# Kernel optimization log

Hardware: AMD Instinct MI355X
Metric: run time of the kernel (lower is better)

The kernel has to match this reference:

```python
import jax, jax.numpy as jnp
import numpy as np

B, S, E, H, D = 4, 2048, 1024, 8, 128
EPS = 1e-5


def _ln(x, g, b):
    m = jnp.mean(x, axis=-1, keepdims=True)
    v = jnp.mean((x - m) ** 2, axis=-1, keepdims=True)
    return (x - m) * jax.lax.rsqrt(v + EPS) * g + b


def _xavier(k, shape, fan_in, fan_out):
    lim = float(np.sqrt(6.0 / (fan_in + fan_out)))
    return jax.random.uniform(k, shape, jnp.float32, -lim, lim)


def setup_inputs() -> dict:
    key = jax.random.key(0)
    ks = jax.random.split(key, 10)
    return {
        "x": jax.random.normal(ks[0], (B, S, E), jnp.float32),
        # embedding_to_z: Linear(E, H*D); stored as [E, H*D] for x @ W
        "W_ez": _xavier(ks[1], (E, H * D), E, H * D),
        "b_ez": jnp.zeros((H * D,), jnp.float32),
        "U_h": _xavier(ks[2], (H, D, D), D, D),
        "U_z": _xavier(ks[3], (H, D, D), D, D),
        "b_u": jnp.zeros((H, D), jnp.float32),
        "out_shaper": _xavier(ks[4], (H, D, D), D, D),
        # shared per-step state LayerNorm
        "lns_g": jnp.ones((D,), jnp.float32),
        "lns_b": jnp.zeros((D,), jnp.float32),
        # per-head FFN: LayerNorm(D) -> Linear(D,D) -> GELU -> Linear(D,E)
        "ff_ln_g": jnp.ones((H, D), jnp.float32),
        "ff_ln_b": jnp.zeros((H, D), jnp.float32),
        "ff_W1": _xavier(ks[5], (H, D, D), D, D),
        "ff_b1": jnp.zeros((H, D), jnp.float32),
        "ff_W2": _xavier(ks[6], (H, D, E), D, E),
        "ff_b2": jnp.zeros((H, E), jnp.float32),
        # layer_attention_weights: Linear(E, 1)
        "w_att": _xavier(ks[7], (E,), E, 1),
        "b_att": jnp.zeros((), jnp.float32),
        # output LayerNorm
        "lno_g": jnp.ones((E,), jnp.float32),
        "lno_b": jnp.zeros((E,), jnp.float32),
    }


def reference(x, W_ez, b_ez, U_h, U_z, b_u, out_shaper, lns_g, lns_b,
              ff_ln_g, ff_ln_b, ff_W1, ff_b1, ff_W2, ff_b2,
              w_att, b_att, lno_g, lno_b):
    b, s, _ = x.shape
    h, d = U_h.shape[0], U_h.shape[1]
    # z tokens: [B,S,H,D]
    z = jnp.tanh((x @ W_ez + b_ez).reshape(b, s, h, d))
    # torch.einsum('bhd,hdd->bhd') takes the DIAGONAL of the second operand
    uh_diag = jnp.einsum('hii->hi', U_h)          # [H,D]
    uz_diag = jnp.einsum('hii->hi', U_z)          # [H,D]
    os_diag = jnp.einsum('hii->hi', out_shaper)   # [H,D]

    def step(h_prev, z_t):
        # h_prev, z_t: [B,H,D]
        u = jax.nn.sigmoid(h_prev * uh_diag + z_t * uz_diag + b_u)
        h_new = u * h_prev + (1.0 - u) * z_t
        h_new = _ln(h_new, lns_g, lns_b)
        return h_new, h_new

    h0 = jnp.zeros((b, h, d), x.dtype)
    _, states = jax.lax.scan(step, h0, jnp.swapaxes(z, 0, 1))  # [S,B,H,D]
    states = jnp.swapaxes(states, 0, 1)                         # [B,S,H,D]

    shaped = states * os_diag                                   # diag einsum
    hln = _ln(shaped, ff_ln_g, ff_ln_b)                         # per-head LN
    h1 = jax.nn.gelu(jnp.einsum('bshd,hde->bshe', hln, ff_W1) + ff_b1,
                     approximate=False)                         # [B,S,H,D]
    ff_out = jnp.einsum('bshd,hde->bshe', h1, ff_W2) + ff_b2    # [B,S,H,E]

    scores = jax.nn.softmax(jnp.einsum('bshe,e->bsh', ff_out, w_att) + b_att,
                            axis=2)                             # over heads
    weighted = jnp.einsum('bshe,bsh->bse', ff_out, scores)      # [B,S,E]
    return _ln(weighted, lno_g, lno_b)
```

## Files before the change

### kernel.cpp

```cpp
#include <hip/hip_runtime.h>
#include <hip/hip_bf16.h>
#include <math.h>

#define BB 4
#define SS 2048
#define EE 1024
#define HH 8
#define DD 128
#define BSR (BB*SS)
#define HD  (HH*DD)
#define LNEPS 1e-5f
#define LOG2E 1.4426950408889634f

#define NCHUNK 16
#define CHS    128
#define NZT    512
#define TPC    64
#define NTICK  (NZT + NCHUNK*TPC)
#define NWORKER 224
#define NSLOT  6
#define SLOTF  (BB*CHS*1024)

#define FSCAN 16
#define FB    32
#define FD    96
#define FE    160
#define FZ    224

typedef __attribute__((ext_vector_type(8))) short bf16x8;
typedef __attribute__((ext_vector_type(4))) float f32x4;

__device__ __forceinline__ ushort f2bf(float f) {
    union { float f; unsigned u; } c{f};
    unsigned r = c.u + 0x7fff + ((c.u >> 16) & 1);
    return (ushort)(r >> 16);
}
__device__ __forceinline__ float bf2f(ushort b) {
    union { unsigned u; float f; } c{(unsigned)b << 16};
    return c.f;
}

typedef __attribute__((address_space(1))) const unsigned int GUI;
typedef __attribute__((address_space(3))) unsigned int LUI;
__device__ __forceinline__ void gl_lds16(const ushort* g, ushort* l) {
    __builtin_amdgcn_global_load_lds((GUI*)g, (LUI*)l, 16, 0, 0);
}

__device__ __forceinline__ float dpp_add(float x, const int ctrl) {
    int y;
    switch (ctrl) {
        case 0x111: y = __builtin_amdgcn_update_dpp(0, __float_as_int(x), 0x111, 0xf, 0xf, true); break;
        case 0x112: y = __builtin_amdgcn_update_dpp(0, __float_as_int(x), 0x112, 0xf, 0xf, true); break;
        case 0x114: y = __builtin_amdgcn_update_dpp(0, __float_as_int(x), 0x114, 0xf, 0xf, true); break;
        case 0x118: y = __builtin_amdgcn_update_dpp(0, __float_as_int(x), 0x118, 0xf, 0xf, true); break;
        case 0x142: y = __builtin_amdgcn_update_dpp(0, __float_as_int(x), 0x142, 0xf, 0xf, true); break;
        default:    y = __builtin_amdgcn_update_dpp(0, __float_as_int(x), 0x143, 0xf, 0xf, true); break;
    }
    return x + __int_as_float(y);
}

__device__ __forceinline__ float wave_sum64(float x) {
    x = dpp_add(x, 0x111);
    x = dpp_add(x, 0x112);
    x = dpp_add(x, 0x114);
    x = dpp_add(x, 0x118);
    x = dpp_add(x, 0x142);
    x = dpp_add(x, 0x143);
    return __int_as_float(__builtin_amdgcn_readlane(__float_as_int(x), 63));
}

__device__ __forceinline__ unsigned flag_peek(unsigned* f) {
    return __hip_atomic_fetch_add(f, 0u, __ATOMIC_RELAXED, __HIP_MEMORY_SCOPE_AGENT);
}
__device__ __forceinline__ void wait_ge(unsigned* f, unsigned tgt) {
    if (threadIdx.x == 0) {
        while (flag_peek(f) < tgt) __builtin_amdgcn_s_sleep(16);
        __builtin_amdgcn_fence(__ATOMIC_ACQUIRE, "agent");
    }
    __syncthreads();
}
__device__ __forceinline__ void wave_wait_ge(unsigned* f, unsigned tgt) {
    unsigned v = 0;
    for (;;) {
        if (threadIdx.x == 0) v = flag_peek(f);
        v = __shfl(v, 0, 64);
        if (v >= tgt) break;
        __builtin_amdgcn_s_sleep(8);
    }
    __builtin_amdgcn_fence(__ATOMIC_ACQUIRE, "agent");
}
__device__ __forceinline__ void done_inc(unsigned* f) {
    __syncthreads();
    if (threadIdx.x == 0) {
        __builtin_amdgcn_fence(__ATOMIC_RELEASE, "agent");
        __hip_atomic_fetch_add(f, 1u, __ATOMIC_RELAXED, __HIP_MEMORY_SCOPE_AGENT);
    }
}
__device__ __forceinline__ unsigned done_inc_ret(unsigned* f, unsigned* sh) {
    __syncthreads();
    if (threadIdx.x == 0) {
        __builtin_amdgcn_fence(__ATOMIC_RELEASE, "agent");
        *sh = __hip_atomic_fetch_add(f, 1u, __ATOMIC_RELAXED, __HIP_MEMORY_SCOPE_AGENT);
    }
    __syncthreads();
    return *sh;
}

__global__ __launch_bounds__(256)
void convx2_k(const float* __restrict__ x,
              ushort* __restrict__ hi, ushort* __restrict__ lo)
{
    const size_t idx = ((size_t)blockIdx.x * 256 + threadIdx.x) * 4;
    const float4 v = *(const float4*)(x + idx);
    ushort4 oh, ol;
    oh.x = f2bf(v.x); ol.x = f2bf(v.x - bf2f(oh.x));
    oh.y = f2bf(v.y); ol.y = f2bf(v.y - bf2f(oh.y));
    oh.z = f2bf(v.z); ol.z = f2bf(v.z - bf2f(oh.z));
    oh.w = f2bf(v.w); ol.w = f2bf(v.w - bf2f(oh.w));
    *(ushort4*)(hi + idx) = oh;
    *(ushort4*)(lo + idx) = ol;
}

__global__ __launch_bounds__(256)
void prepall_k(const float* __restrict__ W_ez,
               ushort* __restrict__ Wth, ushort* __restrict__ Wtl,
               const float* __restrict__ W2, ushort* __restrict__ W2t,
               const float* __restrict__ W1, ushort* __restrict__ W1t,
               const float* __restrict__ w_att, const float* __restrict__ b2,
               const float* __restrict__ b_att,
               const float* __restrict__ Uh, const float* __restrict__ Uz,
               const float* __restrict__ Os,
               float* __restrict__ q, float* __restrict__ c,
               float* __restrict__ uh_d, float* __restrict__ uz_d,
               float* __restrict__ os_d, unsigned* __restrict__ flags)
{
    __shared__ float tile[32][33];
    const int blk = blockIdx.x;
    if (blk == 2434) {
        flags[threadIdx.x] = 0;
        return;
    }
    const int tx = threadIdx.x & 31, ty = threadIdx.x >> 5;
    if (blk < 1024) {
        const int k0 = (blk >> 5) * 32, n0 = (blk & 31) * 32;
        #pragma unroll
        for (int i = 0; i < 4; ++i)
            tile[ty + i*8][tx] = W_ez[(size_t)(k0 + ty + i*8) * 1024 + n0 + tx];
        __syncthreads();
        #pragma unroll
        for (int i = 0; i < 4; ++i) {
            const float v = tile[tx][ty + i*8];
            const ushort h = f2bf(v);
            Wth[(size_t)(n0 + ty + i*8) * 1024 + k0 + tx] = h;
            Wtl[(size_t)(n0 + ty + i*8) * 1024 + k0 + tx] = f2bf(v - bf2f(h));
        }
    } else if (blk < 2048) {
        const int b2i = blk - 1024;
        const int k0 = (b2i >> 5) * 32, n0 = (b2i & 31) * 32;
        #pragma unroll
        for (int i = 0; i < 4; ++i)
            tile[ty + i*8][tx] = W2[(size_t)(k0 + ty + i*8) * 1024 + n0 + tx];
        __syncthreads();
        #pragma unroll
        for (int i = 0; i < 4; ++i)
            W2t[(size_t)(n0 + ty + i*8) * 1024 + k0 + tx] = f2bf(tile[tx][ty + i*8]);
    } else if (blk < 2176) {
        const int idx = blk - 2048;
        const int hh = idx >> 4;
        const int k0 = (idx & 3) * 32, n0 = ((idx >> 2) & 3) * 32;
        const float* Wb = W1 + (size_t)hh * DD * DD;
        ushort*      Wtb = W1t + (size_t)hh * DD * DD;
        #pragma unroll
        for (int i = 0; i < 4; ++i)
            tile[ty + i*8][tx] = Wb[(size_t)(k0 + ty + i*8) * DD + n0 + tx];
        __syncthreads();
        #pragma unroll
        for (int i = 0; i < 4; ++i)
            Wtb[(size_t)(n0 + ty + i*8) * DD + k0 + tx] = f2bf(tile[tx][ty + i*8]);
    } else {
        const int gid  = (blk - 2176) * 256 + threadIdx.x;
        const int wave = gid >> 6, lane = gid & 63;
        if (wave < HD) {
            const float* wp = W2 + (size_t)wave * EE;
            float p = 0.f;
            for (int e = lane; e < EE; e += 64) p = fmaf(wp[e], w_att[e], p);
            #pragma unroll
            for (int off = 32; off > 0; off >>= 1) p += __shfl_xor(p, off, 64);
            if (lane == 0) {
                q[wave] = p;
                const int h = wave >> 7, d = wave & 127;
                uh_d[wave] = Uh[(size_t)h*DD*DD + (size_t)d*DD + d];
                uz_d[wave] = Uz[(size_t)h*DD*DD + (size_t)d*DD + d];
                os_d[wave] = Os[(size_t)h*DD*DD + (size_t)d*DD + d];
            }
        } else if (wave < HD + HH) {
            const int h = wave - HD;
            const float* bp = b2 + (size_t)h * EE;
            float p = 0.f;
            for (int e = lane; e < EE; e += 64) p = fmaf(bp[e], w_att[e], p);
            #pragma unroll
            for (int off = 32; off > 0; off >>= 1) p += __shfl_xor(p, off, 64);
            if (lane == 0) c[h] = p + b_att[0];
        }
    }
}

__global__ __launch_bounds__(256)
void pipeline_k(float* z,
                const ushort* xbh, const ushort* xbl,
                const ushort* __restrict__ Wzh, const ushort* __restrict__ Wzl,
                const float* __restrict__ b_ez,
                const float* __restrict__ uh_d, const float* __restrict__ uz_d,
                const float* __restrict__ b_u,
                const float* __restrict__ lns_g, const float* __restrict__ lns_b,
                ushort* stb,
                const float* __restrict__ os_d,
                const float* __restrict__ ffg, const float* __restrict__ ffb,
                const ushort* __restrict__ W1t, const float* __restrict__ ff_b1,
                const float* __restrict__ qv, const float* __restrict__ cv,
                ushort* __restrict__ h1b, float* __restrict__ logits,
                const ushort* __restrict__ W2t, const float* __restrict__ ff_b2,
                float* __restrict__ wslots,
                const float* __restrict__ lno_g, const float* __restrict__ lno_b,
                float* __restrict__ out,
                unsigned* __restrict__ flags)
{
    __shared__ ushort ldspad[20480];
    if (flags[255] == 0xdeadbeefu)
        ((volatile ushort*)ldspad)[threadIdx.x] = 1;

    if (blockIdx.x < 32) {
        if (threadIdx.x >= 64) return;
        __builtin_amdgcn_s_setprio(3);
        const int bh = blockIdx.x;
        const int b = bh >> 3, h = bh & 7;
        const int l = threadIdx.x;
        const int d0 = 2*l, d1 = d0 + 1;

        const float uhn0 = -uh_d[h*DD+d0] * LOG2E, uhn1 = -uh_d[h*DD+d1] * LOG2E;
        const float uzn0 = -uz_d[h*DD+d0] * LOG2E, uzn1 = -uz_d[h*DD+d1] * LOG2E;
        const float bun0 = -b_u [h*DD+d0] * LOG2E, bun1 = -b_u [h*DD+d1] * LOG2E;
        const float g0  = lns_g[d0], g1 = lns_g[d1];
        const float be0 = lns_b[d0], be1 = lns_b[d1];
        const float A0 = g0 * uhn0, A1 = g1 * uhn1;
        const float bunB0 = fmaf(be0, uhn0, bun0);
        const float bunB1 = fmaf(be1, uhn1, bun1);

        const float* zp = z + ((size_t)b * SS * HH + h) * DD + d0;
        unsigned* op = (unsigned*)(stb + (size_t)b * SS * HD + h * DD) + l;

        wave_wait_ge(&flags[FZ + 0], 32);

        const int CH = 8;
        float2 zc[CH], zn[CH];
        float pb0[CH], pb1[CH];
        #pragma unroll
        for (int i = 0; i < CH; ++i) zc[i] = *(const float2*)(zp + (size_t)i*HD);
        #pragma unroll
        for (int i = 0; i < CH; ++i) {
            pb0[i] = fmaf(zc[i].x, uzn0, bunB0);
            pb1[i] = fmaf(zc[i].y, uzn1, bunB1);
        }

        float r_c, wp0, wp1, W0, W1, dv0, dv1;

#define PACK_STORE(HP0, HP1, OFF) do {                                       \
            const unsigned pu0 = __float_as_uint(HP0) + 0x8000u;             \
            const unsigned pu1 = __float_as_uint(HP1) + 0x8000u;             \
            op[(size_t)(OFF) * (HD/2)] =                                     \
                __builtin_amdgcn_perm(pu1, pu0, 0x07060302u);                \
        } while (0)

#define SCAN_STEP(ZX, ZY, PB0v, PB1v, ZNX, ZNY, OFF) do {                    \
            const float t0 = fmaf(r_c, W0, (PB0v));                          \
            const float t1 = fmaf(r_c, W1, (PB1v));                          \
            const float e0 = __builtin_amdgcn_exp2f(t0);                     \
            const float e1 = __builtin_amdgcn_exp2f(t1);                     \
            const float u0 = __builtin_amdgcn_rcpf(1.f + e0);                \
            const float u1 = __builtin_amdgcn_rcpf(1.f + e1);                \
            const float hn0 = fmaf(u0, dv0, (ZX));                           \
            const float hn1 = fmaf(u1, dv1, (ZY));                           \
            const float s1 = wave_sum64(hn0 + hn1);                          \
            const float s2 = wave_sum64(fmaf(hn0, hn0, hn1*hn1));            \
            const float m   = s1 * (1.f/128.f);                              \
            const float var = fmaf(s2, 1.f/128.f, -m*m);                     \
            r_c = __builtin_amdgcn_rsqf(var + LNEPS);                        \
            wp0 = hn0 - m; wp1 = hn1 - m;                                    \
            W0 = wp0 * A0; W1 = wp1 * A1;                                    \
            const float hp0 = fmaf(wp0, r_c * g0, be0);                      \
            const float hp1 = fmaf(wp1, r_c * g1, be1);                      \
            PACK_STORE(hp0, hp1, OFF);                                       \
            dv0 = hp0 - (ZNX); dv1 = hp1 - (ZNY);                            \
        } while (0)

        {
            const float z0 = zc[0].x, z1 = zc[0].y;
            const float t0 = fmaf(z0, uzn0, bun0);
            const float t1 = fmaf(z1, uzn1, bun1);
            const float e0 = __builtin_amdgcn_exp2f(t0);
            const float e1 = __builtin_amdgcn_exp2f(t1);
            const float u0 = __builtin_amdgcn_rcpf(1.f + e0);
            const float u1 = __builtin_amdgcn_rcpf(1.f + e1);
            const float hn0 = fmaf(u0, -z0, z0);
            const float hn1 = fmaf(u1, -z1, z1);
            const float s1 = wave_sum64(hn0 + hn1);
            const float s2 = wave_sum64(fmaf(hn0, hn0, hn1*hn1));
            const float m   = s1 * (1.f/128.f);
            const float var = fmaf(s2, 1.f/128.f, -m*m);
            r_c = __builtin_amdgcn_rsqf(var + LNEPS);
            wp0 = hn0 - m; wp1 = hn1 - m;
            W0 = wp0 * A0; W1 = wp1 * A1;
            const float hp0 = fmaf(wp0, r_c * g0, be0);
            const float hp1 = fmaf(wp1, r_c * g1, be1);
            PACK_STORE(hp0, hp1, 0);
            dv0 = hp0 - zc[1].x; dv1 = hp1 - zc[1].y;
        }

        #pragma unroll
        for (int i = 0; i < CH; ++i)
            zn[i] = *(const float2*)(zp + (size_t)(CH+i)*HD);
        #pragma unroll
        for (int i = 1; i < CH; ++i) {
            const float znx = (i+1 < CH) ? zc[i+1].x : zn[0].x;
            const float zny = (i+1 < CH) ? zc[i+1].y : zn[0].y;
            SCAN_STEP(zc[i].x, zc[i].y, pb0[i], pb1[i], znx, zny, i);
        }
        #pragma unroll
        for (int i = 0; i < CH; ++i) {
            zc[i] = zn[i];
            pb0[i] = fmaf(zn[i].x, uzn0, bunB0);
            pb1[i] = fmaf(zn[i].y, uzn1, bunB1);
        }

        for (int s0 = CH; s0 < SS; s0 += CH) {
            if (s0 + CH < SS) {
                if (((s0 + CH) & (CHS-1)) == 0)
                    wave_wait_ge(&flags[FZ + ((s0 + CH) >> 7)], 32);
                #pragma unroll
                for (int i = 0; i < CH; ++i)
                    zn[i] = *(const float2*)(zp + (size_t)(s0+CH+i)*HD);
            } else {
                #pragma unroll
                for (int i = 0; i < CH; ++i) zn[i] = make_float2(0.f, 0.f);
            }
            #pragma unroll
            for (int i = 0; i < CH; ++i) {
                const float znx = (i+1 < CH) ? zc[i+1].x : zn[0].x;
                const float zny = (i+1 < CH) ? zc[i+1].y : zn[0].y;
                SCAN_STEP(zc[i].x, zc[i].y, pb0[i], pb1[i], znx, zny, s0 + i);
            }
            #pragma unroll
            for (int i = 0; i < CH; ++i) {
                zc[i] = zn[i];
                pb0[i] = fmaf(zn[i].x, uzn0, bunB0);
                pb1[i] = fmaf(zn[i].y, uzn1, bunB1);
            }
            if ((s0 & (CHS-1)) == CHS - CH) {
                if (threadIdx.x == 0) {
                    __builtin_amdgcn_fence(__ATOMIC_RELEASE, "agent");
                    __hip_atomic_fetch_add(&flags[FSCAN + (s0 >> 7)], 1u,
                                           __ATOMIC_RELAXED, __HIP_MEMORY_SCOPE_AGENT);
                }
            }
        }
#undef SCAN_STEP
#undef PACK_STORE
        return;
    }

    __shared__ ushort ApS[4*128*32];
    __shared__ ushort Bsm[128*32];
    __shared__ float  sLDS[128][8];
    __shared__ float  lpart[128][2];
    __shared__ unsigned s_tk, s_old;
    const int tid = threadIdx.x;
    const int lane = tid & 63, w = tid >> 6;
    const int wr = w >> 1, wc = w & 1;
    const int lr = lane >> 2;
    const int lc = (lane & 3) ^ (lr & 3);
    const int quad = lane >> 4;
    const int fr   = lane & 15;
    const int fchk = (quad ^ (lane & 3)) * 8;

    for (;;) {
        __syncthreads();
        if (tid == 0) s_tk = __hip_atomic_fetch_add(&flags[0], 1u,
                               __ATOMIC_RELAXED, __HIP_MEMORY_SCOPE_AGENT);
        __syncthreads();
        const unsigned tk = s_tk;
        if (tk >= NTICK) return;

        if (tk < NZT) {
            const int zc = (int)(tk >> 5), zb = (int)((tk >> 3) & 3), zy = (int)(tk & 7);
            const int row0 = zb*SS + zc*CHS, col0 = zy*128;
            ushort* AH = ApS;
            ushort* AL = ApS + 4096;
            ushort* BH = ApS + 8192;
            ushort* BL = ApS + 12288;
            const size_t aoff0 = (size_t)(row0 +      w*16 + lr) * 1024 + lc*8;
            const size_t aoff1 = (size_t)(row0 + 64 + w*16 + lr) * 1024 + lc*8;
            const size_t boff0 = (size_t)(col0 +      w*16 + lr) * 1024 + lc*8;
            const size_t boff1 = (size_t)(col0 + 64 + w*16 + lr) * 1024 + lc*8;
            ushort* AH0 = AH + (     w*16) * 32;  ushort* AH1 = AH + (64 + w*16) * 32;
            ushort* AL0 = AL + (     w*16) * 32;  ushort* AL1 = AL + (64 + w*16) * 32;
            ushort* BH0 = BH + (     w*16) * 32;  ushort* BH1 = BH + (64 + w*16) * 32;
            ushort* BL0 = BL + (     w*16) * 32;  ushort* BL1 = BL + (64 + w*16) * 32;

            f32x4 acc[4][4];
            #pragma unroll
            for (int i = 0; i < 4; ++i)
                #pragma unroll
                for (int j = 0; j < 4; ++j) acc[i][j] = (f32x4){0.f,0.f,0.f,0.f};

            for (int k0 = 0; k0 < 1024; k0 += 32) {
                __syncthreads();
                gl_lds16(xbh + aoff0 + k0, AH0);
                gl_lds16(xbh + aoff1 + k0, AH1);
                gl_lds16(Wzh + boff0 + k0, BH0);
                gl_lds16(Wzh + boff1 + k0, BH1);
                gl_lds16(xbl + aoff0 + k0, AL0);
                gl_lds16(xbl + aoff1 + k0, AL1);
                gl_lds16(Wzl + boff0 + k0, BL0);
                gl_lds16(Wzl + boff1 + k0, BL1);
                __syncthreads();

                bf16x8 afh[4], afl[4], bfh[4], bfl[4];
                #pragma unroll
                for (int i = 0; i < 4; ++i) {
                    const int ra = (wr*64 + i*16 + fr) * 32 + fchk;
                    afh[i] = *(const bf16x8*)(AH + ra);
                    afl[i] = *(const bf16x8*)(AL + ra);
                    const int rb = (wc*64 + i*16 + fr) * 32 + fchk;
                    bfh[i] = *(const bf16x8*)(BH + rb);
                    bfl[i] = *(const bf16x8*)(BL + rb);
                }
                #pragma unroll
                for (int i = 0; i < 4; ++i)
                    #pragma unroll
                    for (int j = 0; j < 4; ++j) {
                        acc[i][j] = __builtin_amdgcn_mfma_f32_16x16x32_bf16(
                            afh[i], bfl[j], acc[i][j], 0, 0, 0);
                        acc[i][j] = __builtin_amdgcn_mfma_f32_16x16x32_bf16(
                            afl[i], bfh[j], acc[i][j], 0, 0, 0);
                        acc[i][j] = __builtin_amdgcn_mfma_f32_16x16x32_bf16(
                            afh[i], bfh[j], acc[i][j], 0, 0, 0);
                    }
            }

            float colv[4];
            #pragma unroll
            for (int tj = 0; tj < 4; ++tj)
                colv[tj] = b_ez[col0 + wc*64 + tj*16 + fr];
            #pragma unroll
            for (int ti = 0; ti < 4; ++ti)
                #pragma unroll
                for (int i = 0; i < 4; ++i) {
                    const int row = row0 + wr*64 + ti*16 + quad*4 + i;
                    #pragma unroll
                    for (int tj = 0; tj < 4; ++tj) {
                        const int col = col0 + wc*64 + tj*16 + fr;
                        z[(size_t)row*1024 + col] = tanhf(acc[ti][tj][i] + colv[tj]);
                    }
                }
            done_inc(&flags[FZ + zc]);
            continue;
        }

        const unsigned t2 = tk - NZT;
        const int c = (int)(t2 / TPC);
        const int r = (int)(t2 % TPC);

        if (r < 32) {
            wait_ge(&flags[FSCAN + c], 32);
            const int bb = r >> 3, hh = r & 7;
            const int row0 = bb*SS + c*CHS;

            {
                const int l = lane;
                const int d0 = 2*l, d1 = d0 + 1;
                const float osd0 = os_d[hh*DD + d0], osd1 = os_d[hh*DD + d1];
                const float fg0 = ffg[hh*DD + d0], fg1 = ffg[hh*DD + d1];
                const float fb0 = ffb[hh*DD + d0], fb1 = ffb[hh*DD + d1];
                const unsigned* st_u = (const unsigned*)stb;
                const int p  = l >> 4;
                const int j  = (l >> 2) & 3;
                unsigned* ApU = (unsigned*)ApS;
                for (int it = 0; it < 32; ++it) {
                    const int rloc = it*4 + w;
                    const unsigned v = st_u[(size_t)(row0 + rloc)*512 + hh*64 + l];
                    const float x0 = bf2f((ushort)(v & 0xffff)) * osd0;
                    const float x1 = bf2f((ushort)(v >> 16))    * osd1;
                    float s1 = x0 + x1;
                    float s2 = fmaf(x0, x0, x1*x1);
                    #pragma unroll
                    for (int off = 32; off > 0; off >>= 1) {
                        s1 += __shfl_xor(s1, off, 64);
                        s2 += __shfl_xor(s2, off, 64);
                    }
                    const float m   = s1 * (1.f/128.f);
                    const float var = fmaf(s2, 1.f/128.f, -m*m);
                    const float rr  = rsqrtf(var + LNEPS);
                    const float o0 = fmaf((x0 - m)*rr, fg0, fb0);
                    const float o1 = fmaf((x1 - m)*rr, fg1, fb1);
                    const unsigned pv = (unsigned)f2bf(o0) | ((unsigned)f2bf(o1) << 16);
                    const int js = j ^ (rloc & 3);
                    ApU[p*2048 + rloc*16 + js*4 + (l & 3)] = pv;
                }
            }
            __syncthreads();

            const ushort* Bg0 = W1t + (size_t)hh*DD*DD + (     w*16 + lr) * DD + lc*8;
            const ushort* Bg1 = W1t + (size_t)hh*DD*DD + (64 + w*16 + lr) * DD + lc*8;
            ushort* Bl0 = Bsm + (     w*16) * 32;
            ushort* Bl1 = Bsm + (64 + w*16) * 32;

            f32x4 acc[4][4];
            #pragma unroll
            for (int i = 0; i < 4; ++i)
                #pragma unroll
                for (int j2 = 0; j2 < 4; ++j2) acc[i][j2] = (f32x4){0.f,0.f,0.f,0.f};

            for (int k0 = 0; k0 < 128; k0 += 32) {
                __syncthreads();
                gl_lds16(Bg0 + k0, Bl0);
                gl_lds16(Bg1 + k0, Bl1);
                __syncthreads();

                const ushort* Ap = ApS + (k0 >> 5) * 4096;
                bf16x8 af[4], bf[4];
                #pragma unroll
                for (int i = 0; i < 4; ++i) {
                    af[i] = *(const bf16x8*)(Ap + (wr*64 + i*16 + fr)*32 + fchk);
                    bf[i] = *(const bf16x8*)(Bsm + (wc*64 + i*16 + fr)*32 + fchk);
                }
                #pragma unroll
                for (int i = 0; i < 4; ++i)
                    #pragma unroll
                    for (int j2 = 0; j2 < 4; ++j2)
                        acc[i][j2] = __builtin_amdgcn_mfma_f32_16x16x32_bf16(
                            af[i], bf[j2], acc[i][j2], 0, 0, 0);
            }

            float colv[4], qh[4];
            #pragma unroll
            for (int tj = 0; tj < 4; ++tj) {
                const int col = wc*64 + tj*16 + fr;
                colv[tj] = ff_b1[hh*DD + col];
                qh[tj]   = qv[hh*DD + col];
            }
            #pragma unroll
            for (int ti = 0; ti < 4; ++ti)
                #pragma unroll
                for (int i = 0; i < 4; ++i) {
                    const int row = row0 + wr*64 + ti*16 + quad*4 + i;
                    float p = 0.f;
                    #pragma unroll
                    for (int tj = 0; tj < 4; ++tj) {
                        const int col = wc*64 + tj*16 + fr;
                        float v = acc[ti][tj][i] + colv[tj];
                        v = 0.5f * v * (1.f + erff(v * 0.70710678118654752f));
                        h1b[(size_t)row*1024 + hh*DD + col] = f2bf(v);
                        p = fmaf(v, qh[tj], p);
                    }
                    p = dpp_add(p, 0x111);
                    p = dpp_add(p, 0x112);
                    p = dpp_add(p, 0x114);
                    p = dpp_add(p, 0x118);
                    if (fr == 15)
                        lpart[wr*64 + ti*16 + quad*4 + i][wc] = p;
                }
            __syncthreads();
            if (tid < 128)
                logits[(size_t)(row0 + tid)*HH + hh] = lpart[tid][0] + lpart[tid][1] + cv[hh];
            done_inc(&flags[FB + c*4 + bb]);
        } else {
            const int sub = r - 32;
            const int bb = sub >> 3, cb = sub & 7;
            wait_ge(&flags[FB + c*4 + bb], 8);
            if (c >= NSLOT) wait_ge(&flags[FE + (c-NSLOT)*4 + bb], 1);
            const int row0 = bb*SS + c*CHS, col0 = cb*128;
            float* wslot = wslots + (size_t)(c % NSLOT) * SLOTF;

            if (tid < 128) {
                const float4 l03 = *(const float4*)(logits + (size_t)(row0 + tid)*8);
                const float4 l47 = *(const float4*)(logits + (size_t)(row0 + tid)*8 + 4);
                float lv[8] = {l03.x,l03.y,l03.z,l03.w,l47.x,l47.y,l47.z,l47.w};
                float mx = -1e30f;
                #pragma unroll
                for (int i = 0; i < 8; ++i) mx = fmaxf(mx, lv[i]);
                float den = 0.f;
                #pragma unroll
                for (int i = 0; i < 8; ++i) den += __expf(lv[i] - mx);
                const float rden = 1.f / den;
                #pragma unroll
                for (int i = 0; i < 8; ++i) sLDS[tid][i] = __expf(lv[i] - mx) * rden;
            }
            __syncthreads();

            const ushort* Bg0 = W2t + (size_t)(col0 +      w*16 + lr) * 1024 + lc*8;
            const ushort* Bg1 = W2t + (size_t)(col0 + 64 + w*16 + lr) * 1024 + lc*8;
            ushort* Bl0 = Bsm + (     w*16) * 32;
            ushort* Bl1 = Bsm + (64 + w*16) * 32;
            const int rl0 = w*16 + lr, rl1 = 64 + w*16 + lr;

            f32x4 acc[4][4];
            #pragma unroll
            for (int i = 0; i < 4; ++i)
                #pragma unroll
                for (int j2 = 0; j2 < 4; ++j2) acc[i][j2] = (f32x4){0.f,0.f,0.f,0.f};

            for (int k0 = 0; k0 < 1024; k0 += 32) {
                __syncthreads();
                {
                    const int kk = k0 + lc*8;
                    const int hidx = kk >> 7;
                    bf16x8 a0 = *(const bf16x8*)(h1b + (size_t)(row0 + rl0)*1024 + kk);
                    bf16x8 a1 = *(const bf16x8*)(h1b + (size_t)(row0 + rl1)*1024 + kk);
                    const float sc0 = sLDS[rl0][hidx];
                    const float sc1 = sLDS[rl1][hidx];
                    bf16x8 w0, w1;
                    #pragma unroll
                    for (int e = 0; e < 8; ++e) {
                        w0[e] = (short)f2bf(bf2f((ushort)a0[e]) * sc0);
                        w1[e] = (short)f2bf(bf2f((ushort)a1[e]) * sc1);
                    }
                    *(bf16x8*)(ApS + (     w*16)*32 + lane*8) = w0;
                    *(bf16x8*)(ApS + (64 + w*16)*32 + lane*8) = w1;
                }
                gl_lds16(Bg0 + k0, Bl0);
                gl_lds16(Bg1 + k0, Bl1);
                __syncthreads();

                bf16x8 af[4], bf[4];
                #pragma unroll
                for (int i = 0; i < 4; ++i) {
                    af[i] = *(const bf16x8*)(ApS + (wr*64 + i*16 + fr)*32 + fchk);
                    bf[i] = *(const bf16x8*)(Bsm + (wc*64 + i*16 + fr)*32 + fchk);
                }
                #pragma unroll
                for (int i = 0; i < 4; ++i)
                    #pragma unroll
                    for (int j2 = 0; j2 < 4; ++j2)
                        acc[i][j2] = __builtin_amdgcn_mfma_f32_16x16x32_bf16(
                            af[i], bf[j2], acc[i][j2], 0, 0, 0);
            }

            float b2v[4][HH];
            #pragma unroll
            for (int tj = 0; tj < 4; ++tj) {
                const int col = col0 + wc*64 + tj*16 + fr;
                #pragma unroll
                for (int h = 0; h < HH; ++h) b2v[tj][h] = ff_b2[(size_t)h*EE + col];
            }
            #pragma unroll
            for (int ti = 0; ti < 4; ++ti)
                #pragma unroll
                for (int i = 0; i < 4; ++i) {
                    const int lrow = wr*64 + ti*16 + quad*4 + i;
                    float sc[HH];
                    #pragma unroll
                    for (int h = 0; h < HH; ++h) sc[h] = sLDS[lrow][h];
                    #pragma unroll
                    for (int tj = 0; tj < 4; ++tj) {
                        const int col = col0 + wc*64 + tj*16 + fr;
                        float bbv = 0.f;
                        #pragma unroll
                        for (int h = 0; h < HH; ++h) bbv = fmaf(sc[h], b2v[tj][h], bbv);
                        wslot[(size_t)(bb*128 + lrow)*1024 + col] = acc[ti][tj][i] + bbv;
                    }
                }

            const unsigned old = done_inc_ret(&flags[FD + c*4 + bb], &s_old);
            if (old == 7) {
                if (tid == 0) __builtin_amdgcn_fence(__ATOMIC_ACQUIRE, "agent");
                __syncthreads();
                const float* wsE = wslots + (size_t)(c % NSLOT) * SLOTF
                                 + (size_t)bb * 128 * 1024;
                float4 gvq[4], bvq[4];
                #pragma unroll
                for (int q4 = 0; q4 < 4; ++q4) {
                    gvq[q4] = *(const float4*)(lno_g + lane*4 + q4*256);
                    bvq[q4] = *(const float4*)(lno_b + lane*4 + q4*256);
                }
                for (int it = 0; it < 32; ++it) {
                    const int rloc = it*4 + w;
                    const float* wp = wsE + (size_t)rloc*1024;
                    float4 vq[4];
                    float s1 = 0.f, s2 = 0.f;
                    #pragma unroll
                    for (int q4 = 0; q4 < 4; ++q4) {
                        vq[q4] = *(const float4*)(wp + lane*4 + q4*256);
                        s1 += vq[q4].x + vq[q4].y + vq[q4].z + vq[q4].w;
                        s2 += vq[q4].x*vq[q4].x + vq[q4].y*vq[q4].y
                            + vq[q4].z*vq[q4].z + vq[q4].w*vq[q4].w;
                    }
                    #pragma unroll
                    for (int off = 32; off > 0; off >>= 1) {
                        s1 += __shfl_xor(s1, off, 64);
                        s2 += __shfl_xor(s2, off, 64);
                    }
                    const float m   = s1 * (1.f/1024.f);
                    const float var = fmaf(s2, 1.f/1024.f, -m*m);
                    const float rr  = rsqrtf(var + LNEPS);
                    float* op = out + (size_t)(row0 + rloc)*1024;
                    #pragma unroll
                    for (int q4 = 0; q4 < 4; ++q4) {
                        float4 o;
                        o.x = fmaf((vq[q4].x - m)*rr, gvq[q4].x, bvq[q4].x);
                        o.y = fmaf((vq[q4].y - m)*rr, gvq[q4].y, bvq[q4].y);
                        o.z = fmaf((vq[q4].z - m)*rr, gvq[q4].z, bvq[q4].z);
                        o.w = fmaf((vq[q4].w - m)*rr, gvq[q4].w, bvq[q4].w);
                        *(float4*)(op + lane*4 + q4*256) = o;
                    }
                }
                done_inc(&flags[FE + c*4 + bb]);
            }
        }
    }
}

extern "C" void kernel_launch(void* const* d_in, const int* in_sizes, int n_in,
                              void* d_out, int out_size, void* d_ws, size_t ws_size,
                              hipStream_t stream)
{
    const float* x       = (const float*)d_in[0];
    const float* W_ez    = (const float*)d_in[1];
    const float* b_ez    = (const float*)d_in[2];
    const float* U_h     = (const float*)d_in[3];
    const float* U_z     = (const float*)d_in[4];
    const float* b_u     = (const float*)d_in[5];
    const float* outsh   = (const float*)d_in[6];
    const float* lns_g   = (const float*)d_in[7];
    const float* lns_b   = (const float*)d_in[8];
    const float* ff_ln_g = (const float*)d_in[9];
    const float* ff_ln_b = (const float*)d_in[10];
    const float* ff_W1   = (const float*)d_in[11];
    const float* ff_b1   = (const float*)d_in[12];
    const float* ff_W2   = (const float*)d_in[13];
    const float* ff_b2   = (const float*)d_in[14];
    const float* w_att   = (const float*)d_in[15];
    const float* b_att   = (const float*)d_in[16];
    const float* lno_g   = (const float*)d_in[17];
    const float* lno_b   = (const float*)d_in[18];
    float* out = (float*)d_out;

    float* ws = (float*)d_ws;
    const size_t NBIG = (size_t)BSR * HD;
    float* bufA = ws;
    float* bufB = ws + NBIG;
    float* bufC = ws + 2*NBIG;
    float* ext  = ws + 3*NBIG;
    ushort* W2t   = (ushort*)ext;
    ushort* W1t   = (ushort*)(ext + 512*1024);
    float* logits = ext + 512*1024 + 64*1024;
    float* qv     = logits + BSR*HH;
    float* cv     = qv + HD;
    float* uh_d   = cv + 8;
    float* uz_d   = uh_d + HD;
    float* os_d   = uz_d + HD;
    unsigned* flags = (unsigned*)(os_d + HD);
    ushort* xb_hi = (ushort*)bufB;
    ushort* xb_lo = (ushort*)bufB + NBIG;
    ushort* stb   = (ushort*)bufB;
    ushort* h1b     = (ushort*)bufC;
    float*  wslots  = bufC + 4*1024*1024;
    ushort* WezT_hi = (ushort*)(bufC + 7*1024*1024);
    ushort* WezT_lo = WezT_hi + 1024*1024;

    convx2_k<<<(BSR*EE/4)/256, 256, 0, stream>>>(x, xb_hi, xb_lo);
    prepall_k<<<2435, 256, 0, stream>>>(W_ez, WezT_hi, WezT_lo,
                                        ff_W2, W2t, ff_W1, W1t,
                                        w_att, ff_b2, b_att,
                                        U_h, U_z, outsh,
                                        qv, cv, uh_d, uz_d, os_d, flags);
    pipeline_k<<<32 + NWORKER, 256, 0, stream>>>(
        bufA, xb_hi, xb_lo, WezT_hi, WezT_lo, b_ez,
        uh_d, uz_d, b_u, lns_g, lns_b, stb,
        os_d, ff_ln_g, ff_ln_b,
        W1t, ff_b1, qv, cv, h1b, logits,
        W2t, ff_b2, wslots,
        lno_g, lno_b, out, flags);
}
```

Baseline: 615.8 us.

## Fold input conversion and weight prep into persistent pipeline, use FP32 SIMT z-GEMM

Removes the separate x hi/lo bf16 split kernel and the weight-prep kernel. Weight transposes and the diagonal/q/c precomputation now run as ticks inside the persistent pipeline kernel, and the scan waits on a prep flag. The z projection becomes an FP32 FMA tile GEMM over smaller 32-row tiles, reading x and W_ez directly, and the first chunk is scheduled before the prep work. The intent is to cut launch and conversion traffic and start the serial scan sooner. The cost is giving up the 3-pass bf16 MFMA for scalar FP32 FMAs, which adds arithmetic time per z tile; the slot count also rises from 6 to 8.

```diff
diff --git a/kernel.cpp b/kernel.cpp
--- a/kernel.cpp
+++ b/kernel.cpp
@@ -14,11 +14,13 @@
 
 #define NCHUNK 16
 #define CHS    128
-#define NZT    512
+#define NZ0    128
+#define NPREP  40
+#define ZBASE2 (NZ0+NPREP)
+#define STAGEBASE (ZBASE2 + 15*128)
 #define TPC    64
-#define NTICK  (NZT + NCHUNK*TPC)
-#define NWORKER 224
-#define NSLOT  6
+#define NTICK  (STAGEBASE + NCHUNK*TPC)
+#define NSLOT  8
 #define SLOTF  (BB*CHS*1024)
 
 #define FSCAN 16
@@ -26,6 +28,7 @@
 #define FD    96
 #define FE    160
 #define FZ    224
+#define FP    240
 
 typedef __attribute__((ext_vector_type(8))) short bf16x8;
 typedef __attribute__((ext_vector_type(4))) float f32x4;
@@ -43,6 +46,9 @@
 typedef __attribute__((address_space(1))) const unsigned int GUI;
 typedef __attribute__((address_space(3))) unsigned int LUI;
 __device__ __forceinline__ void gl_lds16(const ushort* g, ushort* l) {
+    __builtin_amdgcn_global_load_lds((GUI*)g, (LUI*)l, 16, 0, 0);
+}
+__device__ __forceinline__ void gl_lds16f(const float* g, float* l) {
     __builtin_amdgcn_global_load_lds((GUI*)g, (LUI*)l, 16, 0, 0);
 }
 
@@ -107,125 +113,35 @@
 }
 
 __global__ __launch_bounds__(256)
-void convx2_k(const float* __restrict__ x,
-              ushort* __restrict__ hi, ushort* __restrict__ lo)
+void zerof_k(unsigned* __restrict__ flags)
 {
-    const size_t idx = ((size_t)blockIdx.x * 256 + threadIdx.x) * 4;
-    const float4 v = *(const float4*)(x + idx);
-    ushort4 oh, ol;
-    oh.x = f2bf(v.x); ol.x = f2bf(v.x - bf2f(oh.x));
-    oh.y = f2bf(v.y); ol.y = f2bf(v.y - bf2f(oh.y));
-    oh.z = f2bf(v.z); ol.z = f2bf(v.z - bf2f(oh.z));
-    oh.w = f2bf(v.w); ol.w = f2bf(v.w - bf2f(oh.w));
-    *(ushort4*)(hi + idx) = oh;
-    *(ushort4*)(lo + idx) = ol;
+    flags[threadIdx.x] = 0;
 }
 
 __global__ __launch_bounds__(256)
-void prepall_k(const float* __restrict__ W_ez,
-               ushort* __restrict__ Wth, ushort* __restrict__ Wtl,
-               const float* __restrict__ W2, ushort* __restrict__ W2t,
-               const float* __restrict__ W1, ushort* __restrict__ W1t,
-               const float* __restrict__ w_att, const float* __restrict__ b2,
-               const float* __restrict__ b_att,
-               const float* __restrict__ Uh, const float* __restrict__ Uz,
-               const float* __restrict__ Os,
-               float* __restrict__ q, float* __restrict__ c,
-               float* __restrict__ uh_d, float* __restrict__ uz_d,
-               float* __restrict__ os_d, unsigned* __restrict__ flags)
-{
-    __shared__ float tile[32][33];
-    const int blk = blockIdx.x;
-    if (blk == 2434) {
-        flags[threadIdx.x] = 0;
-        return;
-    }
-    const int tx = threadIdx.x & 31, ty = threadIdx.x >> 5;
-    if (blk < 1024) {
-        const int k0 = (blk >> 5) * 32, n0 = (blk & 31) * 32;
-        #pragma unroll
-        for (int i = 0; i < 4; ++i)
-            tile[ty + i*8][tx] = W_ez[(size_t)(k0 + ty + i*8) * 1024 + n0 + tx];
-        __syncthreads();
-        #pragma unroll
-        for (int i = 0; i < 4; ++i) {
-            const float v = tile[tx][ty + i*8];
-            const ushort h = f2bf(v);
-            Wth[(size_t)(n0 + ty + i*8) * 1024 + k0 + tx] = h;
-            Wtl[(size_t)(n0 + ty + i*8) * 1024 + k0 + tx] = f2bf(v - bf2f(h));
-        }
-    } else if (blk < 2048) {
-        const int b2i = blk - 1024;
-        const int k0 = (b2i >> 5) * 32, n0 = (b2i & 31) * 32;
-        #pragma unroll
-        for (int i = 0; i < 4; ++i)
-            tile[ty + i*8][tx] = W2[(size_t)(k0 + ty + i*8) * 1024 + n0 + tx];
-        __syncthreads();
-        #pragma unroll
-        for (int i = 0; i < 4; ++i)
-            W2t[(size_t)(n0 + ty + i*8) * 1024 + k0 + tx] = f2bf(tile[tx][ty + i*8]);
-    } else if (blk < 2176) {
-        const int idx = blk - 2048;
-        const int hh = idx >> 4;
-        const int k0 = (idx & 3) * 32, n0 = ((idx >> 2) & 3) * 32;
-        const float* Wb = W1 + (size_t)hh * DD * DD;
-        ushort*      Wtb = W1t + (size_t)hh * DD * DD;
-        #pragma unroll
-        for (int i = 0; i < 4; ++i)
-            tile[ty + i*8][tx] = Wb[(size_t)(k0 + ty + i*8) * DD + n0 + tx];
-        __syncthreads();
-        #pragma unroll
-        for (int i = 0; i < 4; ++i)
-            Wtb[(size_t)(n0 + ty + i*8) * DD + k0 + tx] = f2bf(tile[tx][ty + i*8]);
-    } else {
-        const int gid  = (blk - 2176) * 256 + threadIdx.x;
-        const int wave = gid >> 6, lane = gid & 63;
-        if (wave < HD) {
-            const float* wp = W2 + (size_t)wave * EE;
-            float p = 0.f;
-            for (int e = lane; e < EE; e += 64) p = fmaf(wp[e], w_att[e], p);
-            #pragma unroll
-            for (int off = 32; off > 0; off >>= 1) p += __shfl_xor(p, off, 64);
-            if (lane == 0) {
-                q[wave] = p;
-                const int h = wave >> 7, d = wave & 127;
-                uh_d[wave] = Uh[(size_t)h*DD*DD + (size_t)d*DD + d];
-                uz_d[wave] = Uz[(size_t)h*DD*DD + (size_t)d*DD + d];
-                os_d[wave] = Os[(size_t)h*DD*DD + (size_t)d*DD + d];
-            }
-        } else if (wave < HD + HH) {
-            const int h = wave - HD;
-            const float* bp = b2 + (size_t)h * EE;
-            float p = 0.f;
-            for (int e = lane; e < EE; e += 64) p = fmaf(bp[e], w_att[e], p);
-            #pragma unroll
-            for (int off = 32; off > 0; off >>= 1) p += __shfl_xor(p, off, 64);
-            if (lane == 0) c[h] = p + b_att[0];
-        }
-    }
-}
-
-__global__ __launch_bounds__(256)
-void pipeline_k(float* z,
-                const ushort* xbh, const ushort* xbl,
-                const ushort* __restrict__ Wzh, const ushort* __restrict__ Wzl,
-                const float* __restrict__ b_ez,
-                const float* __restrict__ uh_d, const float* __restrict__ uz_d,
+void pipeline_k(float* __restrict__ z,
+                const float* __restrict__ xg,
+                const float* __restrict__ Wez, const float* __restrict__ b_ez,
+                const float* __restrict__ W2, const float* __restrict__ W1,
+                const float* __restrict__ w_att, const float* __restrict__ b_att,
+                const float* __restrict__ Uh, const float* __restrict__ Uz,
+                const float* __restrict__ Os,
                 const float* __restrict__ b_u,
                 const float* __restrict__ lns_g, const float* __restrict__ lns_b,
-                ushort* stb,
-                const float* __restrict__ os_d,
+                ushort* __restrict__ stb,
                 const float* __restrict__ ffg, const float* __restrict__ ffb,
-                const ushort* __restrict__ W1t, const float* __restrict__ ff_b1,
-                const float* __restrict__ qv, const float* __restrict__ cv,
+                ushort* __restrict__ W1t, const float* __restrict__ ff_b1,
+                float* __restrict__ qv, float* __restrict__ cv,
+                float* __restrict__ uh_d, float* __restrict__ uz_d,
+                float* __restrict__ os_d,
                 ushort* __restrict__ h1b, float* __restrict__ logits,
-                const ushort* __restrict__ W2t, const float* __restrict__ ff_b2,
+                ushort* __restrict__ W2t, const float* __restrict__ ff_b2,
                 float* __restrict__ wslots,
                 const float* __restrict__ lno_g, const float* __restrict__ lno_b,
                 float* __restrict__ out,
                 unsigned* __restrict__ flags)
 {
-    __shared__ ushort ldspad[20480];
+    __shared__ ushort ldspad[11520];
     if (flags[255] == 0xdeadbeefu)
         ((volatile ushort*)ldspad)[threadIdx.x] = 1;
 
@@ -236,6 +152,8 @@
         const int b = bh >> 3, h = bh & 7;
         const int l = threadIdx.x;
         const int d0 = 2*l, d1 = d0 + 1;
+
+        wave_wait_ge(&flags[FP], NPREP);
 
         const float uhn0 = -uh_d[h*DD+d0] * LOG2E, uhn1 = -uh_d[h*DD+d1] * LOG2E;
         const float uzn0 = -uz_d[h*DD+d0] * LOG2E, uzn1 = -uz_d[h*DD+d1] * LOG2E;
@@ -249,7 +167,7 @@
         const float* zp = z + ((size_t)b * SS * HH + h) * DD + d0;
         unsigned* op = (unsigned*)(stb + (size_t)b * SS * HD + h * DD) + l;
 
-        wave_wait_ge(&flags[FZ + 0], 32);
+        wave_wait_ge(&flags[FZ + 0], 128);
 
         const int CH = 8;
         float2 zc[CH], zn[CH];
@@ -262,7 +180,7 @@
             pb1[i] = fmaf(zc[i].y, uzn1, bunB1);
         }
 
-        float r_c, wp0, wp1, W0, W1, dv0, dv1;
+        float r_c, wp0, wp1, W0, W1r, dv0, dv1;
 
 #define PACK_STORE(HP0, HP1, OFF) do {                                       \
             const unsigned pu0 = __float_as_uint(HP0) + 0x8000u;             \
@@ -273,7 +191,7 @@
 
 #define SCAN_STEP(ZX, ZY, PB0v, PB1v, ZNX, ZNY, OFF) do {                    \
             const float t0 = fmaf(r_c, W0, (PB0v));                          \
-            const float t1 = fmaf(r_c, W1, (PB1v));                          \
+            const float t1 = fmaf(r_c, W1r, (PB1v));                         \
             const float e0 = __builtin_amdgcn_exp2f(t0);                     \
             const float e1 = __builtin_amdgcn_exp2f(t1);                     \
             const float u0 = __builtin_amdgcn_rcpf(1.f + e0);                \
@@ -286,7 +204,7 @@
             const float var = fmaf(s2, 1.f/128.f, -m*m);                     \
             r_c = __builtin_amdgcn_rsqf(var + LNEPS);                        \
             wp0 = hn0 - m; wp1 = hn1 - m;                                    \
-            W0 = wp0 * A0; W1 = wp1 * A1;                                    \
+            W0 = wp0 * A0; W1r = wp1 * A1;                                   \
             const float hp0 = fmaf(wp0, r_c * g0, be0);                      \
             const float hp1 = fmaf(wp1, r_c * g1, be1);                      \
             PACK_STORE(hp0, hp1, OFF);                                       \
@@ -309,7 +227,7 @@
             const float var = fmaf(s2, 1.f/128.f, -m*m);
             r_c = __builtin_amdgcn_rsqf(var + LNEPS);
             wp0 = hn0 - m; wp1 = hn1 - m;
-            W0 = wp0 * A0; W1 = wp1 * A1;
+            W0 = wp0 * A0; W1r = wp1 * A1;
             const float hp0 = fmaf(wp0, r_c * g0, be0);
             const float hp1 = fmaf(wp1, r_c * g1, be1);
             PACK_STORE(hp0, hp1, 0);
@@ -335,7 +253,7 @@
         for (int s0 = CH; s0 < SS; s0 += CH) {
             if (s0 + CH < SS) {
                 if (((s0 + CH) & (CHS-1)) == 0)
-                    wave_wait_ge(&flags[FZ + ((s0 + CH) >> 7)], 32);
+                    wave_wait_ge(&flags[FZ + ((s0 + CH) >> 7)], 128);
                 #pragma unroll
                 for (int i = 0; i < CH; ++i)
                     zn[i] = *(const float2*)(zp + (size_t)(s0+CH+i)*HD);
@@ -372,6 +290,8 @@
     __shared__ ushort Bsm[128*32];
     __shared__ float  sLDS[128][8];
     __shared__ float  lpart[128][2];
+    __shared__ float  xtile[32][68];
+    __shared__ float  ttile[32][33];
     __shared__ unsigned s_tk, s_old;
     const int tid = threadIdx.x;
     const int lane = tid & 63, w = tid >> 6;
@@ -390,83 +310,152 @@
         const unsigned tk = s_tk;
         if (tk >= NTICK) return;
 
-        if (tk < NZT) {
-            const int zc = (int)(tk >> 5), zb = (int)((tk >> 3) & 3), zy = (int)(tk & 7);
-            const int row0 = zb*SS + zc*CHS, col0 = zy*128;
-            ushort* AH = ApS;
-            ushort* AL = ApS + 4096;
-            ushort* BH = ApS + 8192;
-            ushort* BL = ApS + 12288;
-            const size_t aoff0 = (size_t)(row0 +      w*16 + lr) * 1024 + lc*8;
-            const size_t aoff1 = (size_t)(row0 + 64 + w*16 + lr) * 1024 + lc*8;
-            const size_t boff0 = (size_t)(col0 +      w*16 + lr) * 1024 + lc*8;
-            const size_t boff1 = (size_t)(col0 + 64 + w*16 + lr) * 1024 + lc*8;
-            ushort* AH0 = AH + (     w*16) * 32;  ushort* AH1 = AH + (64 + w*16) * 32;
-            ushort* AL0 = AL + (     w*16) * 32;  ushort* AL1 = AL + (64 + w*16) * 32;
-            ushort* BH0 = BH + (     w*16) * 32;  ushort* BH1 = BH + (64 + w*16) * 32;
-            ushort* BL0 = BL + (     w*16) * 32;  ushort* BL1 = BL + (64 + w*16) * 32;
-
-            f32x4 acc[4][4];
-            #pragma unroll
-            for (int i = 0; i < 4; ++i)
-                #pragma unroll
-                for (int j = 0; j < 4; ++j) acc[i][j] = (f32x4){0.f,0.f,0.f,0.f};
-
-            for (int k0 = 0; k0 < 1024; k0 += 32) {
+        if (tk < STAGEBASE && !(tk >= NZ0 && tk < ZBASE2)) {
+            int c, idx;
+            if (tk < NZ0) { c = 0; idx = (int)tk; }
+            else { const int zt = (int)tk - NPREP; c = zt >> 7; idx = zt & 127; }
+            const int bb = idx >> 5, rsub = (idx >> 3) & 3, cb = idx & 7;
+            const int row0 = bb*SS + c*CHS + rsub*32;
+            const int col0 = cb*128;
+            const int rg = tid >> 4, cg = tid & 15;
+
+            float a0[8], a1[8];
+            #pragma unroll
+            for (int j = 0; j < 8; ++j) { a0[j] = 0.f; a1[j] = 0.f; }
+            float (*Wt)[128] = (float(*)[128])ApS;
+
+            const int fi  = (lane & 31) * 4;
+            const int cgS = (fi & 63) >> 2;
+            const int jo  = (fi >> 6) * 4;
+
+            for (int kb = 0; kb < 1024; kb += 64) {
                 __syncthreads();
-                gl_lds16(xbh + aoff0 + k0, AH0);
-                gl_lds16(xbh + aoff1 + k0, AH1);
-                gl_lds16(Wzh + boff0 + k0, BH0);
-                gl_lds16(Wzh + boff1 + k0, BH1);
-                gl_lds16(xbl + aoff0 + k0, AL0);
-                gl_lds16(xbl + aoff1 + k0, AL1);
-                gl_lds16(Wzl + boff0 + k0, BL0);
-                gl_lds16(Wzl + boff1 + k0, BL1);
+                {
+                    const int xr = tid >> 3, xk = (tid & 7) * 8;
+                    const float* xs = xg + (size_t)(row0 + xr)*1024 + kb + xk;
+                    const float4 va = *(const float4*)(xs);
+                    const float4 vb = *(const float4*)(xs + 4);
+                    *(float4*)&xtile[xr][xk]     = va;
+                    *(float4*)&xtile[xr][xk + 4] = vb;
+                }
+                {
+                    float* dstbase = &Wt[0][0] + (size_t)w * 2048;
+                    #pragma unroll
+                    for (int j = 0; j < 8; ++j) {
+                        const int li = w*8 + j;
+                        const int kk = li*2 + (lane >> 5);
+                        gl_lds16f(Wez + (size_t)(kb + kk)*1024 + col0 + cgS*8 + jo,
+                                  dstbase + j*256);
+                    }
+                }
                 __syncthreads();
-
-                bf16x8 afh[4], afl[4], bfh[4], bfl[4];
-                #pragma unroll
-                for (int i = 0; i < 4; ++i) {
-                    const int ra = (wr*64 + i*16 + fr) * 32 + fchk;
-                    afh[i] = *(const bf16x8*)(AH + ra);
-                    afl[i] = *(const bf16x8*)(AL + ra);
-                    const int rb = (wc*64 + i*16 + fr) * 32 + fchk;
-                    bfh[i] = *(const bf16x8*)(BH + rb);
-                    bfl[i] = *(const bf16x8*)(BL + rb);
-                }
-                #pragma unroll
-                for (int i = 0; i < 4; ++i)
-                    #pragma unroll
-                    for (int j = 0; j < 4; ++j) {
-                        acc[i][j] = __builtin_amdgcn_mfma_f32_16x16x32_bf16(
-                            afh[i], bfl[j], acc[i][j], 0, 0, 0);
-                        acc[i][j] = __builtin_amdgcn_mfma_f32_16x16x32_bf16(
-                            afl[i], bfh[j], acc[i][j], 0, 0, 0);
-                        acc[i][j] = __builtin_amdgcn_mfma_f32_16x16x32_bf16(
-                            afh[i], bfh[j], acc[i][j], 0, 0, 0);
-                    }
-            }
-
-            float colv[4];
-            #pragma unroll
-            for (int tj = 0; tj < 4; ++tj)
-                colv[tj] = b_ez[col0 + wc*64 + tj*16 + fr];
-            #pragma unroll
-            for (int ti = 0; ti < 4; ++ti)
-                #pragma unroll
-                for (int i = 0; i < 4; ++i) {
-                    const int row = row0 + wr*64 + ti*16 + quad*4 + i;
-                    #pragma unroll
-                    for (int tj = 0; tj < 4; ++tj) {
-                        const int col = col0 + wc*64 + tj*16 + fr;
-                        z[(size_t)row*1024 + col] = tanhf(acc[ti][tj][i] + colv[tj]);
-                    }
-                }
-            done_inc(&flags[FZ + zc]);
+                #pragma unroll 8
+                for (int kk = 0; kk < 64; ++kk) {
+                    const float x0 = xtile[rg*2][kk];
+                    const float x1 = xtile[rg*2 + 1][kk];
+                    const float4 wa = *(const float4*)&Wt[kk][cg*4];
+                    const float4 wb = *(const float4*)&Wt[kk][64 + cg*4];
+                    a0[0] = fmaf(x0, wa.x, a0[0]);  a1[0] = fmaf(x1, wa.x, a1[0]);
+                    a0[1] = fmaf(x0, wa.y, a0[1]);  a1[1] = fmaf(x1, wa.y, a1[1]);
+                    a0[2] = fmaf(x0, wa.z, a0[2]);  a1[2] = fmaf(x1, wa.z, a1[2]);
+                    a0[3] = fmaf(x0, wa.w, a0[3]);  a1[3] = fmaf(x1, wa.w, a1[3]);
+                    a0[4] = fmaf(x0, wb.x, a0[4]);  a1[4] = fmaf(x1, wb.x, a1[4]);
+                    a0[5] = fmaf(x0, wb.y, a0[5]);  a1[5] = fmaf(x1, wb.y, a1[5]);
+                    a0[6] = fmaf(x0, wb.z, a0[6]);  a1[6] = fmaf(x1, wb.z, a1[6]);
+                    a0[7] = fmaf(x0, wb.w, a0[7]);  a1[7] = fmaf(x1, wb.w, a1[7]);
+                }
+            }
+            {
+                const int zcol = col0 + cg*8;
+                const float4 bza = *(const float4*)(b_ez + zcol);
+                const float4 bzb = *(const float4*)(b_ez + zcol + 4);
+                float* zr0 = z + (size_t)(row0 + rg*2)*1024 + zcol;
+                float4 o;
+                o.x = tanhf(a0[0]+bza.x); o.y = tanhf(a0[1]+bza.y);
+                o.z = tanhf(a0[2]+bza.z); o.w = tanhf(a0[3]+bza.w);
+                *(float4*)(zr0) = o;
+                o.x = tanhf(a0[4]+bzb.x); o.y = tanhf(a0[5]+bzb.y);
+                o.z = tanhf(a0[6]+bzb.z); o.w = tanhf(a0[7]+bzb.w);
+                *(float4*)(zr0 + 4) = o;
+                o.x = tanhf(a1[0]+bza.x); o.y = tanhf(a1[1]+bza.y);
+                o.z = tanhf(a1[2]+bza.z); o.w = tanhf(a1[3]+bza.w);
+                *(float4*)(zr0 + 1024) = o;
+                o.x = tanhf(a1[4]+bzb.x); o.y = tanhf(a1[5]+bzb.y);
+                o.z = tanhf(a1[6]+bzb.z); o.w = tanhf(a1[7]+bzb.w);
+                *(float4*)(zr0 + 1028) = o;
+            }
+            done_inc(&flags[FZ + c]);
             continue;
         }
 
-        const unsigned t2 = tk - NZT;
+        if (tk < ZBASE2) {
+            const int p = (int)tk - NZ0;
+            const int tx = tid & 31, ty = tid >> 5;
+            if (p < 32) {
+                for (int i5 = 0; i5 < 32; ++i5) {
+                    const int t2i = p*32 + i5;
+                    const int k0 = (t2i >> 5) * 32, n0 = (t2i & 31) * 32;
+                    __syncthreads();
+                    #pragma unroll
+                    for (int ii = 0; ii < 4; ++ii)
+                        ttile[ty + ii*8][tx] = W2[(size_t)(k0 + ty + ii*8)*1024 + n0 + tx];
+                    __syncthreads();
+                    #pragma unroll
+                    for (int ii = 0; ii < 4; ++ii)
+                        W2t[(size_t)(n0 + ty + ii*8)*1024 + k0 + tx] =
+                            f2bf(ttile[tx][ty + ii*8]);
+                }
+            } else if (p < 36) {
+                for (int i5 = 0; i5 < 32; ++i5) {
+                    const int idx = (p - 32)*32 + i5;
+                    const int hh = idx >> 4;
+                    const int k0 = (idx & 3)*32, n0 = ((idx >> 2) & 3)*32;
+                    const float* Wb = W1 + (size_t)hh * DD * DD;
+                    ushort*     Wtb = W1t + (size_t)hh * DD * DD;
+                    __syncthreads();
+                    #pragma unroll
+                    for (int ii = 0; ii < 4; ++ii)
+                        ttile[ty + ii*8][tx] = Wb[(size_t)(k0 + ty + ii*8)*DD + n0 + tx];
+                    __syncthreads();
+                    #pragma unroll
+                    for (int ii = 0; ii < 4; ++ii)
+                        Wtb[(size_t)(n0 + ty + ii*8)*DD + k0 + tx] =
+                            f2bf(ttile[tx][ty + ii*8]);
+                }
+            } else {
+                const int base = (p - 36) * 258;
+                for (int it = 0; it < 65; ++it) {
+                    const int wv = base + it*4 + w;
+                    if (wv >= base + 258 || wv >= HD + HH) continue;
+                    if (wv < HD) {
+                        const float* wp = W2 + (size_t)wv * EE;
+                        float pp = 0.f;
+                        for (int e = lane; e < EE; e += 64) pp = fmaf(wp[e], w_att[e], pp);
+                        #pragma unroll
+                        for (int off = 32; off > 0; off >>= 1) pp += __shfl_xor(pp, off, 64);
+                        if (lane == 0) {
+                            qv[wv] = pp;
+                            const int hq = wv >> 7, dq = wv & 127;
+                            uh_d[wv] = Uh[(size_t)hq*DD*DD + (size_t)dq*DD + dq];
+                            uz_d[wv] = Uz[(size_t)hq*DD*DD + (size_t)dq*DD + dq];
+                            os_d[wv] = Os[(size_t)hq*DD*DD + (size_t)dq*DD + dq];
+                        }
+                    } else {
+                        const int hq = wv - HD;
+                        const float* bp = ff_b2 + (size_t)hq * EE;
+                        float pp = 0.f;
+                        for (int e = lane; e < EE; e += 64) pp = fmaf(bp[e], w_att[e], pp);
+                        #pragma unroll
+                        for (int off = 32; off > 0; off >>= 1) pp += __shfl_xor(pp, off, 64);
+                        if (lane == 0) cv[hq] = pp + b_att[0];
+                    }
+                }
+            }
+            done_inc(&flags[FP]);
+            continue;
+        }
+
+        const unsigned t2 = tk - STAGEBASE;
         const int c = (int)(t2 / TPC);
         const int r = (int)(t2 % TPC);
 
@@ -759,25 +748,15 @@
     float* uz_d   = uh_d + HD;
     float* os_d   = uz_d + HD;
     unsigned* flags = (unsigned*)(os_d + HD);
-    ushort* xb_hi = (ushort*)bufB;
-    ushort* xb_lo = (ushort*)bufB + NBIG;
     ushort* stb   = (ushort*)bufB;
-    ushort* h1b     = (ushort*)bufC;
-    float*  wslots  = bufC + 4*1024*1024;
-    ushort* WezT_hi = (ushort*)(bufC + 7*1024*1024);
-    ushort* WezT_lo = WezT_hi + 1024*1024;
-
-    convx2_k<<<(BSR*EE/4)/256, 256, 0, stream>>>(x, xb_hi, xb_lo);
-    prepall_k<<<2435, 256, 0, stream>>>(W_ez, WezT_hi, WezT_lo,
-                                        ff_W2, W2t, ff_W1, W1t,
-                                        w_att, ff_b2, b_att,
-                                        U_h, U_z, outsh,
-                                        qv, cv, uh_d, uz_d, os_d, flags);
-    pipeline_k<<<32 + NWORKER, 256, 0, stream>>>(
-        bufA, xb_hi, xb_lo, WezT_hi, WezT_lo, b_ez,
-        uh_d, uz_d, b_u, lns_g, lns_b, stb,
-        os_d, ff_ln_g, ff_ln_b,
-        W1t, ff_b1, qv, cv, h1b, logits,
-        W2t, ff_b2, wslots,
+    ushort* h1b   = (ushort*)bufC;
+    float*  wslots = bufC + 4*1024*1024;
+
+    zerof_k<<<1, 256, 0, stream>>>(flags);
+    pipeline_k<<<256, 256, 0, stream>>>(
+        bufA, x, W_ez, b_ez, ff_W2, ff_W1, w_att, b_att,
+        U_h, U_z, outsh, b_u, lns_g, lns_b, stb,
+        ff_ln_g, ff_ln_b, W1t, ff_b1, qv, cv, uh_d, uz_d, os_d,
+        h1b, logits, W2t, ff_b2, wslots,
         lno_g, lno_b, out, flags);
 }
```

Result: slower. 927.8 us (+50.7%).
